# Kernel tuning notes

Measured on AMD Instinct MI355X. Metric: run time of the kernel, lower is better.

## Reference

```python
import jax, jax.numpy as jnp
import numpy as np


def setup_inputs() -> dict:
    key = jax.random.key(0)
    ks = jax.random.split(key, 8)
    B = 32768
    return {
        "x": jax.random.normal(ks[0], (B, 784), dtype=jnp.float32),
        "conv_w": jax.random.normal(ks[1], (3, 3), dtype=jnp.float32),
        "fc1_w": jax.random.normal(ks[2], (512, 676), dtype=jnp.float32) * 0.04,
        "fc1_b": jax.random.normal(ks[3], (512,), dtype=jnp.float32),
        "fc2_w": jax.random.normal(ks[4], (512, 512), dtype=jnp.float32) * 0.04,
        "fc2_b": jax.random.normal(ks[5], (512,), dtype=jnp.float32),
        "out_w": jax.random.normal(ks[6], (10, 512), dtype=jnp.float32) * 0.04,
        "out_b": jax.random.normal(ks[7], (10,), dtype=jnp.float32),
    }


def reference(x, conv_w, fc1_w, fc1_b, fc2_w, fc2_b, out_w, out_b):
    B = x.shape[0]
    img = x.reshape(B, 1, 28, 28)  # NCHW, single channel
    # Valid 3x3 cross-correlation (same math as the nested tensordot loop).
    kern = conv_w.reshape(1, 1, 3, 3)  # OIHW
    conv = jax.lax.conv_general_dilated(
        img, kern, window_strides=(1, 1), padding="VALID",
        dimension_numbers=("NCHW", "OIHW", "NCHW"))  # [B,1,26,26]
    h = conv.reshape(B, 26 * 26)
    h = jax.nn.relu(h @ fc1_w.T + fc1_b)
    h = jax.nn.relu(h @ fc2_w.T + fc2_b)
    return h @ out_w.T + out_b  # [B,10] logits
```

## Files before the change

### kernel.cpp

```cpp
#include <hip/hip_runtime.h>

typedef unsigned short ushort_t;
typedef __attribute__((ext_vector_type(8))) short bf16x8;
typedef __attribute__((ext_vector_type(4))) float f32x4;
typedef __attribute__((ext_vector_type(16))) float f32x16;

__device__ __forceinline__ unsigned short f2bf(float f) {
    union { float f; unsigned u; } v; v.f = f;
    unsigned r = v.u + 0x7FFFu + ((v.u >> 16) & 1u);
    return (unsigned short)(r >> 16);
}

__global__ __launch_bounds__(256) void prep_w(const float* __restrict__ fc1_w,
                                              const float* __restrict__ cw,
                                              const float* __restrict__ fc2_w,
                                              const float* __restrict__ out_w,
                                              ushort_t* __restrict__ W1,
                                              ushort_t* __restrict__ W2,
                                              ushort_t* __restrict__ W3) {
    const int idx = blockIdx.x * 256 + threadIdx.x;
    if (idx < 425984) {
        const int ngrp = idx / 26624;
        const int kfrag = (idx % 26624) >> 9;
        const int li = idx & 511;
        const int lane = li >> 3, e = li & 7;
        const int n = ngrp * 32 + (lane & 31);
        const int p = kfrag * 16 + (lane >> 5) * 8 + e;
        float acc = 0.f;
        if (p < 784) {
            const int pr = p / 28, pc = p % 28;
#pragma unroll
            for (int dr = 0; dr < 3; ++dr) {
                const int r = pr - dr;
                if (r < 0 || r >= 26) continue;
#pragma unroll
                for (int dc = 0; dc < 3; ++dc) {
                    const int col = pc - dc;
                    if (col < 0 || col >= 26) continue;
                    acc += cw[dr * 3 + dc] * fc1_w[n * 676 + r * 26 + col];
                }
            }
        }
        W1[idx] = f2bf(acc);
    }
    if (idx < 262144) {
        const int ngrp = idx / 16384;
        const int kfrag = (idx % 16384) >> 9;
        const int li = idx & 511;
        const int lane = li >> 3, e = li & 7;
        const int n = ngrp * 32 + (lane & 31);
        const int p = kfrag * 16 + (lane >> 5) * 8 + e;
        W2[idx] = f2bf(fc2_w[n * 512 + p]);
    }
    if (idx < 16 * 512)  W3[idx] = (idx < 10 * 512) ? f2bf(out_w[idx]) : (ushort_t)0;
}

__global__ __launch_bounds__(512, 4) void mega5(const float* __restrict__ x,
                                                const ushort_t* __restrict__ W1,
                                                const ushort_t* __restrict__ W2,
                                                const ushort_t* __restrict__ W3,
                                                const float* __restrict__ b1,
                                                const float* __restrict__ b2,
                                                const float* __restrict__ ob,
                                                float* __restrict__ out) {
    extern __shared__ ushort_t smem[];
    ushort_t* xs0 = smem;
    ushort_t* hs  = smem + 4096;

    const int tid = threadIdx.x;
    const int wave = tid >> 6, lane = tid & 63;
    const int r32 = lane & 31, khalf = lane >> 5;
    const int xrow = tid >> 3, xoct = tid & 7;
    const int m0 = blockIdx.x * 64;
    const size_t ng0 = wave * 2, ng1 = wave * 2 + 1;

    f32x16 acc[2][2];
#pragma unroll
    for (int a = 0; a < 2; ++a)
#pragma unroll
        for (int j = 0; j < 2; ++j)
#pragma unroll
            for (int e = 0; e < 16; ++e) acc[a][j][e] = 0.f;

    f32x4 xv0, xv1;
    auto load_x = [&](int ks) {
        const int gc = ks * 64 + xoct * 8;
        if (gc < 784) {
            const f32x4* p = (const f32x4*)&x[(size_t)(m0 + xrow) * 784 + gc];
            xv0 = __builtin_nontemporal_load(p);
            xv1 = __builtin_nontemporal_load(p + 1);
        } else {
            xv0 = (f32x4){0.f, 0.f, 0.f, 0.f};
            xv1 = (f32x4){0.f, 0.f, 0.f, 0.f};
        }
    };
    auto store_x = [&](ushort_t* buf) {
        bf16x8 xv;
        xv[0] = (short)f2bf(xv0.x); xv[1] = (short)f2bf(xv0.y);
        xv[2] = (short)f2bf(xv0.z); xv[3] = (short)f2bf(xv0.w);
        xv[4] = (short)f2bf(xv1.x); xv[5] = (short)f2bf(xv1.y);
        xv[6] = (short)f2bf(xv1.z); xv[7] = (short)f2bf(xv1.w);
        *(bf16x8*)&buf[xrow * 64 + ((xoct ^ (xrow & 7)) * 8)] = xv;
    };

    auto write_h = [&](const float* __restrict__ bias) {
#pragma unroll
        for (int j = 0; j < 2; ++j) {
            const int n = (wave * 2 + j) * 32 + r32;
            const float bb = bias[n];
            const int nseg = n >> 3, nrem = n & 7;
#pragma unroll
            for (int i = 0; i < 2; ++i)
#pragma unroll
                for (int reg = 0; reg < 16; ++reg) {
                    const int m = i * 32 + 4 * khalf + (reg & 3) + 8 * (reg >> 2);
                    hs[m * 512 + ((nseg ^ (m & 7)) * 8) + nrem] = f2bf(fmaxf(acc[i][j][reg] + bb, 0.f));
                }
        }
    };

    load_x(0);
    store_x(xs0);
    __syncthreads();

    for (int ks = 0; ks < 12; ++ks) {
        load_x(ks + 1);
        const ushort_t* bufp = (ks & 1) ? hs : xs0;
#pragma unroll
        for (int ksub = 0; ksub < 4; ++ksub) {
            const int kfrag = ks * 4 + ksub;
            const bf16x8 bw0 = *(const bf16x8*)&W1[(ng0 * 52 + kfrag) * 512 + lane * 8];
            const bf16x8 bw1 = *(const bf16x8*)&W1[(ng1 * 52 + kfrag) * 512 + lane * 8];
            const int q = 2 * ksub + khalf;
            bf16x8 af[2];
#pragma unroll
            for (int i = 0; i < 2; ++i) {
                const int m = i * 32 + r32;
                af[i] = *(const bf16x8*)&bufp[m * 64 + ((q ^ (m & 7)) * 8)];
            }
            __builtin_amdgcn_s_setprio(1);
            acc[0][0] = __builtin_amdgcn_mfma_f32_32x32x16_bf16(af[0], bw0, acc[0][0], 0, 0, 0);
            acc[0][1] = __builtin_amdgcn_mfma_f32_32x32x16_bf16(af[0], bw1, acc[0][1], 0, 0, 0);
            acc[1][0] = __builtin_amdgcn_mfma_f32_32x32x16_bf16(af[1], bw0, acc[1][0], 0, 0, 0);
            acc[1][1] = __builtin_amdgcn_mfma_f32_32x32x16_bf16(af[1], bw1, acc[1][1], 0, 0, 0);
            __builtin_amdgcn_s_setprio(0);
        }
        store_x((ks & 1) ? xs0 : hs);
        __syncthreads();
    }
    {
        const ushort_t* bufp = xs0;
        const int kfrag = 48;
        const bf16x8 bw0 = *(const bf16x8*)&W1[(ng0 * 52 + kfrag) * 512 + lane * 8];
        const bf16x8 bw1 = *(const bf16x8*)&W1[(ng1 * 52 + kfrag) * 512 + lane * 8];
        const int q = khalf;
        bf16x8 af[2];
#pragma unroll
        for (int i = 0; i < 2; ++i) {
            const int m = i * 32 + r32;
            af[i] = *(const bf16x8*)&bufp[m * 64 + ((q ^ (m & 7)) * 8)];
        }
        __builtin_amdgcn_s_setprio(1);
        acc[0][0] = __builtin_amdgcn_mfma_f32_32x32x16_bf16(af[0], bw0, acc[0][0], 0, 0, 0);
        acc[0][1] = __builtin_amdgcn_mfma_f32_32x32x16_bf16(af[0], bw1, acc[0][1], 0, 0, 0);
        acc[1][0] = __builtin_amdgcn_mfma_f32_32x32x16_bf16(af[1], bw0, acc[1][0], 0, 0, 0);
        acc[1][1] = __builtin_amdgcn_mfma_f32_32x32x16_bf16(af[1], bw1, acc[1][1], 0, 0, 0);
        __builtin_amdgcn_s_setprio(0);
    }

    write_h(b1);
#pragma unroll
    for (int a = 0; a < 2; ++a)
#pragma unroll
        for (int j = 0; j < 2; ++j)
#pragma unroll
            for (int e = 0; e < 16; ++e) acc[a][j][e] = 0.f;
    __syncthreads();

    for (int ks = 0; ks < 8; ++ks) {
#pragma unroll
        for (int ksub = 0; ksub < 4; ++ksub) {
            const int kfrag = ks * 4 + ksub;
            const bf16x8 bw0 = *(const bf16x8*)&W2[(ng0 * 32 + kfrag) * 512 + lane * 8];
            const bf16x8 bw1 = *(const bf16x8*)&W2[(ng1 * 32 + kfrag) * 512 + lane * 8];
            const int hq = ks * 8 + 2 * ksub + khalf;
            bf16x8 af[2];
#pragma unroll
            for (int i = 0; i < 2; ++i) {
                const int m = i * 32 + r32;
                af[i] = *(const bf16x8*)&hs[m * 512 + ((hq ^ (m & 7)) * 8)];
            }
            __builtin_amdgcn_s_setprio(1);
            acc[0][0] = __builtin_amdgcn_mfma_f32_32x32x16_bf16(af[0], bw0, acc[0][0], 0, 0, 0);
            acc[0][1] = __builtin_amdgcn_mfma_f32_32x32x16_bf16(af[0], bw1, acc[0][1], 0, 0, 0);
            acc[1][0] = __builtin_amdgcn_mfma_f32_32x32x16_bf16(af[1], bw0, acc[1][0], 0, 0, 0);
            acc[1][1] = __builtin_amdgcn_mfma_f32_32x32x16_bf16(af[1], bw1, acc[1][1], 0, 0, 0);
            __builtin_amdgcn_s_setprio(0);
        }
    }
    __syncthreads();

    write_h(b2);
    __syncthreads();

    if (wave < 4) {
        const int quad = lane >> 4, l16 = lane & 15;
        const int row = wave * 16 + l16;
        f32x4 hacc = {0.f, 0.f, 0.f, 0.f};
#pragma unroll
        for (int ks = 0; ks < 16; ++ks) {
            const int seg = 4 * ks + quad;
            const bf16x8 a = *(const bf16x8*)&hs[row * 512 + ((seg ^ (row & 7)) * 8)];
            const bf16x8 b = *(const bf16x8*)&W3[l16 * 512 + ks * 32 + quad * 8];
            hacc = __builtin_amdgcn_mfma_f32_16x16x32_bf16(a, b, hacc, 0, 0, 0);
        }
        if (l16 < 10) {
            const float bb = ob[l16];
#pragma unroll
            for (int r = 0; r < 4; ++r)
                out[(size_t)(m0 + wave * 16 + quad * 4 + r) * 10 + l16] = hacc[r] + bb;
        }
    }
}

extern "C" void kernel_launch(void* const* d_in, const int* in_sizes, int n_in,
                              void* d_out, int out_size, void* d_ws, size_t ws_size,
                              hipStream_t stream) {
    const float* x      = (const float*)d_in[0];
    const float* conv_w = (const float*)d_in[1];
    const float* fc1_w  = (const float*)d_in[2];
    const float* fc1_b  = (const float*)d_in[3];
    const float* fc2_w  = (const float*)d_in[4];
    const float* fc2_b  = (const float*)d_in[5];
    const float* out_w  = (const float*)d_in[6];
    const float* out_b  = (const float*)d_in[7];
    float* out = (float*)d_out;

    ushort_t* W1 = (ushort_t*)d_ws;
    ushort_t* W2 = W1 + 425984;
    ushort_t* W3 = W2 + 262144;

    prep_w<<<dim3(1664), 256, 0, stream>>>(fc1_w, conv_w, fc2_w, out_w, W1, W2, W3);

    mega5<<<dim3(512), 512, 73728, stream>>>(x, W1, W2, W3, fc1_b, fc2_b, out_b, out);
}
```

Before: 216.8 us.

## Software-pipeline weight fragment loads and use packed bf16 conversion

Result: no change. 214.8 us (-0.9%).

```diff
diff --git a/kernel.cpp b/kernel.cpp
--- a/kernel.cpp
+++ b/kernel.cpp
@@ -9,6 +9,12 @@
     union { float f; unsigned u; } v; v.f = f;
     unsigned r = v.u + 0x7FFFu + ((v.u >> 16) & 1u);
     return (unsigned short)(r >> 16);
+}
+
+__device__ __forceinline__ unsigned cvt_pk_bf16(float a, float b) {
+    unsigned r;
+    asm("v_cvt_pk_bf16_f32 %0, %1, %2" : "=v"(r) : "v"(a), "v"(b));
+    return r;
 }
 
 __global__ __launch_bounds__(256) void prep_w(const float* __restrict__ fc1_w,
@@ -29,15 +35,19 @@
         float acc = 0.f;
         if (p < 784) {
             const int pr = p / 28, pc = p % 28;
+            const float* frow = &fc1_w[n * 676];
 #pragma unroll
             for (int dr = 0; dr < 3; ++dr) {
                 const int r = pr - dr;
-                if (r < 0 || r >= 26) continue;
+                const bool rok = (unsigned)r < 26u;
+                const int rc = rok ? r : 0;
 #pragma unroll
                 for (int dc = 0; dc < 3; ++dc) {
-                    const int col = pc - dc;
-                    if (col < 0 || col >= 26) continue;
-                    acc += cw[dr * 3 + dc] * fc1_w[n * 676 + r * 26 + col];
+                    const int c = pc - dc;
+                    const bool cok = (unsigned)c < 26u;
+                    const int cc = cok ? c : 0;
+                    const float w = (rok && cok) ? cw[dr * 3 + dc] : 0.f;
+                    acc += w * frow[rc * 26 + cc];
                 }
             }
         }
@@ -55,14 +65,14 @@
     if (idx < 16 * 512)  W3[idx] = (idx < 10 * 512) ? f2bf(out_w[idx]) : (ushort_t)0;
 }
 
-__global__ __launch_bounds__(512, 4) void mega5(const float* __restrict__ x,
-                                                const ushort_t* __restrict__ W1,
-                                                const ushort_t* __restrict__ W2,
-                                                const ushort_t* __restrict__ W3,
-                                                const float* __restrict__ b1,
-                                                const float* __restrict__ b2,
-                                                const float* __restrict__ ob,
-                                                float* __restrict__ out) {
+__global__ __launch_bounds__(512, 4) void mega13(const float* __restrict__ x,
+                                                 const ushort_t* __restrict__ W1,
+                                                 const ushort_t* __restrict__ W2,
+                                                 const ushort_t* __restrict__ W3,
+                                                 const float* __restrict__ b1,
+                                                 const float* __restrict__ b2,
+                                                 const float* __restrict__ ob,
+                                                 float* __restrict__ out) {
     extern __shared__ ushort_t smem[];
     ushort_t* xs0 = smem;
     ushort_t* hs  = smem + 4096;
@@ -73,6 +83,11 @@
     const int xrow = tid >> 3, xoct = tid & 7;
     const int m0 = blockIdx.x * 64;
     const size_t ng0 = wave * 2, ng1 = wave * 2 + 1;
+
+    const ushort_t* w1p0 = &W1[ng0 * 52 * 512 + lane * 8];
+    const ushort_t* w1p1 = &W1[ng1 * 52 * 512 + lane * 8];
+    const ushort_t* w2p0 = &W2[ng0 * 32 * 512 + lane * 8];
+    const ushort_t* w2p1 = &W2[ng1 * 32 * 512 + lane * 8];
 
     f32x16 acc[2][2];
 #pragma unroll
@@ -95,12 +110,11 @@
         }
     };
     auto store_x = [&](ushort_t* buf) {
-        bf16x8 xv;
-        xv[0] = (short)f2bf(xv0.x); xv[1] = (short)f2bf(xv0.y);
-        xv[2] = (short)f2bf(xv0.z); xv[3] = (short)f2bf(xv0.w);
-        xv[4] = (short)f2bf(xv1.x); xv[5] = (short)f2bf(xv1.y);
-        xv[6] = (short)f2bf(xv1.z); xv[7] = (short)f2bf(xv1.w);
-        *(bf16x8*)&buf[xrow * 64 + ((xoct ^ (xrow & 7)) * 8)] = xv;
+        union { bf16x8 h; unsigned u[4]; } a, b;
+        a.u[0] = cvt_pk_bf16(xv0.x, xv0.y); a.u[1] = cvt_pk_bf16(xv0.z, xv0.w);
+        a.u[2] = cvt_pk_bf16(xv1.x, xv1.y); a.u[3] = cvt_pk_bf16(xv1.z, xv1.w);
+        (void)b;
+        *(bf16x8*)&buf[xrow * 64 + ((xoct ^ (xrow & 7)) * 8)] = a.h;
     };
 
     auto write_h = [&](const float* __restrict__ bias) {
@@ -123,14 +137,23 @@
     store_x(xs0);
     __syncthreads();
 
+    bf16x8 bwc0 = *(const bf16x8*)(w1p0);
+    bf16x8 bwc1 = *(const bf16x8*)(w1p1);
+
     for (int ks = 0; ks < 12; ++ks) {
         load_x(ks + 1);
         const ushort_t* bufp = (ks & 1) ? hs : xs0;
 #pragma unroll
         for (int ksub = 0; ksub < 4; ++ksub) {
-            const int kfrag = ks * 4 + ksub;
-            const bf16x8 bw0 = *(const bf16x8*)&W1[(ng0 * 52 + kfrag) * 512 + lane * 8];
-            const bf16x8 bw1 = *(const bf16x8*)&W1[(ng1 * 52 + kfrag) * 512 + lane * 8];
+            const int kf = ks * 4 + ksub;
+            bf16x8 bwn0, bwn1;
+            if (kf < 48) {
+                bwn0 = *(const bf16x8*)(w1p0 + (kf + 1) * 512);
+                bwn1 = *(const bf16x8*)(w1p1 + (kf + 1) * 512);
+            } else {
+                bwn0 = *(const bf16x8*)(w2p0);
+                bwn1 = *(const bf16x8*)(w2p1);
+            }
             const int q = 2 * ksub + khalf;
             bf16x8 af[2];
 #pragma unroll
@@ -139,20 +162,20 @@
                 af[i] = *(const bf16x8*)&bufp[m * 64 + ((q ^ (m & 7)) * 8)];
             }
             __builtin_amdgcn_s_setprio(1);
-            acc[0][0] = __builtin_amdgcn_mfma_f32_32x32x16_bf16(af[0], bw0, acc[0][0], 0, 0, 0);
-            acc[0][1] = __builtin_amdgcn_mfma_f32_32x32x16_bf16(af[0], bw1, acc[0][1], 0, 0, 0);
-            acc[1][0] = __builtin_amdgcn_mfma_f32_32x32x16_bf16(af[1], bw0, acc[1][0], 0, 0, 0);
-            acc[1][1] = __builtin_amdgcn_mfma_f32_32x32x16_bf16(af[1], bw1, acc[1][1], 0, 0, 0);
+            acc[0][0] = __builtin_amdgcn_mfma_f32_32x32x16_bf16(af[0], bwc0, acc[0][0], 0, 0, 0);
+            acc[0][1] = __builtin_amdgcn_mfma_f32_32x32x16_bf16(af[0], bwc1, acc[0][1], 0, 0, 0);
+            acc[1][0] = __builtin_amdgcn_mfma_f32_32x32x16_bf16(af[1], bwc0, acc[1][0], 0, 0, 0);
+            acc[1][1] = __builtin_amdgcn_mfma_f32_32x32x16_bf16(af[1], bwc1, acc[1][1], 0, 0, 0);
             __builtin_amdgcn_s_setprio(0);
+            bwc0 = bwn0; bwc1 = bwn1;
         }
         store_x((ks & 1) ? xs0 : hs);
         __syncthreads();
     }
     {
         const ushort_t* bufp = xs0;
-        const int kfrag = 48;
-        const bf16x8 bw0 = *(const bf16x8*)&W1[(ng0 * 52 + kfrag) * 512 + lane * 8];
-        const bf16x8 bw1 = *(const bf16x8*)&W1[(ng1 * 52 + kfrag) * 512 + lane * 8];
+        bf16x8 bwn0 = *(const bf16x8*)(w2p0);
+        bf16x8 bwn1 = *(const bf16x8*)(w2p1);
         const int q = khalf;
         bf16x8 af[2];
 #pragma unroll
@@ -161,11 +184,12 @@
             af[i] = *(const bf16x8*)&bufp[m * 64 + ((q ^ (m & 7)) * 8)];
         }
         __builtin_amdgcn_s_setprio(1);
-        acc[0][0] = __builtin_amdgcn_mfma_f32_32x32x16_bf16(af[0], bw0, acc[0][0], 0, 0, 0);
-        acc[0][1] = __builtin_amdgcn_mfma_f32_32x32x16_bf16(af[0], bw1, acc[0][1], 0, 0, 0);
-        acc[1][0] = __builtin_amdgcn_mfma_f32_32x32x16_bf16(af[1], bw0, acc[1][0], 0, 0, 0);
-        acc[1][1] = __builtin_amdgcn_mfma_f32_32x32x16_bf16(af[1], bw1, acc[1][1], 0, 0, 0);
+        acc[0][0] = __builtin_amdgcn_mfma_f32_32x32x16_bf16(af[0], bwc0, acc[0][0], 0, 0, 0);
+        acc[0][1] = __builtin_amdgcn_mfma_f32_32x32x16_bf16(af[0], bwc1, acc[0][1], 0, 0, 0);
+        acc[1][0] = __builtin_amdgcn_mfma_f32_32x32x16_bf16(af[1], bwc0, acc[1][0], 0, 0, 0);
+        acc[1][1] = __builtin_amdgcn_mfma_f32_32x32x16_bf16(af[1], bwc1, acc[1][1], 0, 0, 0);
         __builtin_amdgcn_s_setprio(0);
+        bwc0 = bwn0; bwc1 = bwn1;
     }
 
     write_h(b1);
@@ -180,10 +204,13 @@
     for (int ks = 0; ks < 8; ++ks) {
 #pragma unroll
         for (int ksub = 0; ksub < 4; ++ksub) {
-            const int kfrag = ks * 4 + ksub;
-            const bf16x8 bw0 = *(const bf16x8*)&W2[(ng0 * 32 + kfrag) * 512 + lane * 8];
-            const bf16x8 bw1 = *(const bf16x8*)&W2[(ng1 * 32 + kfrag) * 512 + lane * 8];
-            const int hq = ks * 8 + 2 * ksub + khalf;
+            const int kf = ks * 4 + ksub;
+            bf16x8 bwn0, bwn1;
+            if (kf < 31) {
+                bwn0 = *(const bf16x8*)(w2p0 + (kf + 1) * 512);
+                bwn1 = *(const bf16x8*)(w2p1 + (kf + 1) * 512);
+            }
+            const int hq = kf * 2 + khalf;
             bf16x8 af[2];
 #pragma unroll
             for (int i = 0; i < 2; ++i) {
@@ -191,11 +218,12 @@
                 af[i] = *(const bf16x8*)&hs[m * 512 + ((hq ^ (m & 7)) * 8)];
             }
             __builtin_amdgcn_s_setprio(1);
-            acc[0][0] = __builtin_amdgcn_mfma_f32_32x32x16_bf16(af[0], bw0, acc[0][0], 0, 0, 0);
-            acc[0][1] = __builtin_amdgcn_mfma_f32_32x32x16_bf16(af[0], bw1, acc[0][1], 0, 0, 0);
-            acc[1][0] = __builtin_amdgcn_mfma_f32_32x32x16_bf16(af[1], bw0, acc[1][0], 0, 0, 0);
-            acc[1][1] = __builtin_amdgcn_mfma_f32_32x32x16_bf16(af[1], bw1, acc[1][1], 0, 0, 0);
+            acc[0][0] = __builtin_amdgcn_mfma_f32_32x32x16_bf16(af[0], bwc0, acc[0][0], 0, 0, 0);
+            acc[0][1] = __builtin_amdgcn_mfma_f32_32x32x16_bf16(af[0], bwc1, acc[0][1], 0, 0, 0);
+            acc[1][0] = __builtin_amdgcn_mfma_f32_32x32x16_bf16(af[1], bwc0, acc[1][0], 0, 0, 0);
+            acc[1][1] = __builtin_amdgcn_mfma_f32_32x32x16_bf16(af[1], bwc1, acc[1][1], 0, 0, 0);
             __builtin_amdgcn_s_setprio(0);
+            if (kf < 31) { bwc0 = bwn0; bwc1 = bwn1; }
         }
     }
     __syncthreads();
@@ -242,5 +270,5 @@
 
     prep_w<<<dim3(1664), 256, 0, stream>>>(fc1_w, conv_w, fc2_w, out_w, W1, W2, W3);
 
-    mega5<<<dim3(512), 512, 73728, stream>>>(x, W1, W2, W3, fc1_b, fc2_b, out_b, out);
-}
+    mega13<<<dim3(512), 512, 73728, stream>>>(x, W1, W2, W3, fc1_b, fc2_b, out_b, out);
+}
```
